# Kernel optimization log

Hardware: AMD Instinct MI355X
Metric: run time of the kernel (lower is better)

The kernel has to match this reference:

```python
import jax, jax.numpy as jnp
import numpy as np

RBF_RADIUS = 12.0
NUM_GAUSSIANS = 50
NUM_ELEMENTS = 100
NUM_MASKS = 1
NUM_HEADS = 8
N_NODES = 50000
N_EDGES = 1000000


def setup_inputs() -> dict:
    key = jax.random.key(0)
    k1, k2, k3, k4 = jax.random.split(key, 4)
    anum = jax.random.randint(k1, (N_NODES,), 0, NUM_ELEMENTS)
    edge_index = jax.random.randint(k2, (2, N_EDGES), 0, N_NODES)
    dist = jax.random.uniform(k3, (N_EDGES,), dtype=jnp.float32) * RBF_RADIUS
    embedding = jax.random.normal(
        k4, (NUM_ELEMENTS, NUM_ELEMENTS, NUM_MASKS, NUM_HEADS, NUM_GAUSSIANS),
        dtype=jnp.float32)
    return {"anum": anum, "edge_index": edge_index, "dist": dist,
            "embedding": embedding}


def _gaussian_smearing(dist):
    # offsets evenly spaced on [0, rbf_radius], std = rbf_radius / num_gaussians
    offsets = jnp.linspace(0.0, RBF_RADIUS, NUM_GAUSSIANS, dtype=jnp.float32)
    std = RBF_RADIUS / NUM_GAUSSIANS
    coeff = -0.5 / (std * std)
    diff = dist[:, None] - offsets[None, :]          # [E, G]
    return jnp.exp(coeff * diff * diff)              # [E, G]


def reference(anum, edge_index, dist, embedding):
    rbf = _gaussian_smearing(dist)                   # [E, G]
    src = anum[edge_index[0]]                        # [E]
    dst = anum[edge_index[1]]                        # [E]
    alphas = embedding[src, dst]                     # [E, M, H, G]
    # einsum 'ijkl,il->jik': i=edges, j=masks, k=heads, l=gaussians
    attn_bias = jnp.einsum('emhg,eg->meh', alphas, rbf)  # [M, E, H]
    return attn_bias
```

## Files before the change

kernel.cpp:

```cpp
#include <hip/hip_runtime.h>


#define G_NUM 50
#define H_NUM 8
#define NE_NUM 100
#define N_PAIRS (NE_NUM * NE_NUM)
#define WIN 16
#define BLOCK_THREADS 256
#define EDGES_PER_BLOCK 128

#define SPACING (12.0f / (float)(G_NUM - 1))
#define INV_SPACING ((float)(G_NUM - 1) / 12.0f)
#define RBF_COEFF (-0.5f * ((float)G_NUM / 12.0f) * ((float)G_NUM / 12.0f))

__global__ __launch_bounds__(BLOCK_THREADS) void transpose_cast_kernel(
    const float* __restrict__ emb, unsigned short* __restrict__ temb)
{
    int idx = blockIdx.x * BLOCK_THREADS + threadIdx.x;
    if (idx < N_PAIRS * H_NUM * G_NUM) {
        int p = idx / (H_NUM * G_NUM);
        int r = idx - p * (H_NUM * G_NUM);
        int g = r >> 3;
        int h = r & 7;
        float f = emb[p * (H_NUM * G_NUM) + h * G_NUM + g];
        unsigned u = __float_as_uint(f);
        unsigned rnd = (u + 0x7fffu + ((u >> 16) & 1u)) >> 16;
        temb[idx] = (unsigned short)rnd;
    }
}

__global__ __launch_bounds__(BLOCK_THREADS) void gather_kernel(
    const int* __restrict__ anum,
    const int* __restrict__ edge_index,
    const float* __restrict__ dist,
    const unsigned short* __restrict__ temb,
    float* __restrict__ out,
    int n_edges)
{
    __shared__ int   pb_s[EDGES_PER_BLOCK];
    __shared__ float dv_s[EDGES_PER_BLOCK];

    const int tid = threadIdx.x;
    const int e0  = blockIdx.x * EDGES_PER_BLOCK;

    if (tid < EDGES_PER_BLOCK) {
        int e = e0 + tid;
        if (e >= n_edges) e = n_edges - 1;
        int s = edge_index[e];
        int d = edge_index[n_edges + e];
        pb_s[tid] = (anum[s] * NE_NUM + anum[d]) * (H_NUM * G_NUM);
        dv_s[tid] = dist[e];
    }
    __syncthreads();

    const int el = tid >> 1;
    const int j  = tid & 1;
    const float dv = dv_s[el];

    int g0 = (int)(dv * INV_SPACING) - 7;
    if (g0 < 0) g0 = 0;
    if (g0 > G_NUM - WIN) g0 = G_NUM - WIN;

    const unsigned short* wb = temb + pb_s[el] + g0 * H_NUM;

    float a0 = 0.f, a1 = 0.f, a2 = 0.f, a3 = 0.f;
    float a4 = 0.f, a5 = 0.f, a6 = 0.f, a7 = 0.f;
    #pragma unroll
    for (int k = 0; k < WIN / 2; ++k) {
        int row = 2 * k + j;
        uint4 v = *(const uint4*)(wb + row * H_NUM);
        float diff = dv - (float)(g0 + row) * SPACING;
        float rb = __expf(RBF_COEFF * diff * diff);
        a0 += rb * __uint_as_float(v.x << 16);
        a1 += rb * __uint_as_float(v.x & 0xffff0000u);
        a2 += rb * __uint_as_float(v.y << 16);
        a3 += rb * __uint_as_float(v.y & 0xffff0000u);
        a4 += rb * __uint_as_float(v.z << 16);
        a5 += rb * __uint_as_float(v.z & 0xffff0000u);
        a6 += rb * __uint_as_float(v.w << 16);
        a7 += rb * __uint_as_float(v.w & 0xffff0000u);
    }

    a0 += __shfl_xor(a0, 1); a1 += __shfl_xor(a1, 1);
    a2 += __shfl_xor(a2, 1); a3 += __shfl_xor(a3, 1);
    a4 += __shfl_xor(a4, 1); a5 += __shfl_xor(a5, 1);
    a6 += __shfl_xor(a6, 1); a7 += __shfl_xor(a7, 1);

    int e = e0 + el;
    if (e < n_edges) {
        float4 w = j ? make_float4(a4, a5, a6, a7) : make_float4(a0, a1, a2, a3);
        *(float4*)(out + (size_t)e * H_NUM + 4 * j) = w;
    }
}

__global__ __launch_bounds__(BLOCK_THREADS) void direct_kernel(
    const int* __restrict__ anum,
    const int* __restrict__ edge_index,
    const float* __restrict__ dist,
    const float* __restrict__ emb,
    float* __restrict__ out,
    int n_edges)
{
    __shared__ int   pair_s[32];
    __shared__ float dist_sd[32];
    __shared__ float rbf_sd[32 * G_NUM];

    const int tid = threadIdx.x;
    const int e0  = blockIdx.x * 32;

    if (tid < 32) {
        int e = e0 + tid;
        if (e >= n_edges) e = n_edges - 1;
        int s  = edge_index[e];
        int d  = edge_index[n_edges + e];
        pair_s[tid] = (anum[s] * NE_NUM + anum[d]) * (H_NUM * G_NUM);
        dist_sd[tid] = dist[e];
    }
    __syncthreads();

    for (int idx = tid; idx < 32 * G_NUM; idx += BLOCK_THREADS) {
        int el = idx / G_NUM;
        int g  = idx - el * G_NUM;
        float diff = dist_sd[el] - (float)g * SPACING;
        rbf_sd[idx] = __expf(RBF_COEFF * diff * diff);
    }
    __syncthreads();

    const int el = tid >> 3;
    const int h  = tid & 7;
    const float* ebase = emb + pair_s[el] + h * G_NUM;
    const float* rbase = rbf_sd + el * G_NUM;

    float acc = 0.0f;
    #pragma unroll
    for (int g2 = 0; g2 < G_NUM / 2; ++g2) {
        float2 ev = *(const float2*)(ebase + 2 * g2);
        float2 rv = *(const float2*)(rbase + 2 * g2);
        acc += ev.x * rv.x + ev.y * rv.y;
    }

    if (e0 + el < n_edges)
        out[e0 * H_NUM + tid] = acc;
}

extern "C" void kernel_launch(void* const* d_in, const int* in_sizes, int n_in,
                              void* d_out, int out_size, void* d_ws, size_t ws_size,
                              hipStream_t stream) {
    const int*   anum       = (const int*)d_in[0];
    const int*   edge_index = (const int*)d_in[1];
    const float* dist       = (const float*)d_in[2];
    const float* emb        = (const float*)d_in[3];
    float*       out        = (float*)d_out;
    const int n_edges = in_sizes[2];

    const size_t temb_bytes = (size_t)N_PAIRS * H_NUM * G_NUM * sizeof(unsigned short);

    if (ws_size < temb_bytes) {
        const int grid = (n_edges + 31) / 32;
        direct_kernel<<<grid, BLOCK_THREADS, 0, stream>>>(
            anum, edge_index, dist, emb, out, n_edges);
        return;
    }

    unsigned short* temb = (unsigned short*)d_ws;

    const int tgrid = (N_PAIRS * H_NUM * G_NUM + BLOCK_THREADS - 1) / BLOCK_THREADS;
    transpose_cast_kernel<<<tgrid, BLOCK_THREADS, 0, stream>>>(emb, temb);

    const int grid = (n_edges + EDGES_PER_BLOCK - 1) / EDGES_PER_BLOCK;
    gather_kernel<<<grid, BLOCK_THREADS, 0, stream>>>(
        anum, edge_index, dist, temb, out, n_edges);
}
```

Baseline: 131.5 us.

## Narrow gaussian window, use one thread per edge, stage transpose through shared memory

The truncated gaussian window in the gather shrinks from 16 to 8 rows. Each thread now handles a whole edge and loads all 8 rows up front, which removes the per-edge thread pair and the shuffle reduction. The transpose-and-cast kernel now stages 8 pairs per block in shared memory with coalesced float4 reads and writes two packed bf16 values per 32-bit store, replacing the strided global reads. The narrower window drops gaussian terms about 3.5 standard deviations out, adding a small approximation error on top of the bf16 rounding.

```diff
diff --git a/kernel.cpp b/kernel.cpp
--- a/kernel.cpp
+++ b/kernel.cpp
@@ -5,27 +5,45 @@
 #define H_NUM 8
 #define NE_NUM 100
 #define N_PAIRS (NE_NUM * NE_NUM)
-#define WIN 16
+#define WIN 8
 #define BLOCK_THREADS 256
-#define EDGES_PER_BLOCK 128
+#define TP_PAIRS 8
 
 #define SPACING (12.0f / (float)(G_NUM - 1))
 #define INV_SPACING ((float)(G_NUM - 1) / 12.0f)
 #define RBF_COEFF (-0.5f * ((float)G_NUM / 12.0f) * ((float)G_NUM / 12.0f))
 
+__device__ __forceinline__ float bf_lo(unsigned u) { return __uint_as_float(u << 16); }
+__device__ __forceinline__ float bf_hi(unsigned u) { return __uint_as_float(u & 0xffff0000u); }
+
 __global__ __launch_bounds__(BLOCK_THREADS) void transpose_cast_kernel(
-    const float* __restrict__ emb, unsigned short* __restrict__ temb)
+    const float* __restrict__ emb, unsigned int* __restrict__ temb)
 {
-    int idx = blockIdx.x * BLOCK_THREADS + threadIdx.x;
-    if (idx < N_PAIRS * H_NUM * G_NUM) {
-        int p = idx / (H_NUM * G_NUM);
-        int r = idx - p * (H_NUM * G_NUM);
-        int g = r >> 3;
-        int h = r & 7;
-        float f = emb[p * (H_NUM * G_NUM) + h * G_NUM + g];
-        unsigned u = __float_as_uint(f);
-        unsigned rnd = (u + 0x7fffu + ((u >> 16) & 1u)) >> 16;
-        temb[idx] = (unsigned short)rnd;
+    __shared__ float ls[TP_PAIRS * H_NUM * G_NUM];
+
+    const int tid = threadIdx.x;
+    const int p0  = blockIdx.x * TP_PAIRS;
+
+    const float4* src = (const float4*)(emb + (size_t)p0 * (H_NUM * G_NUM));
+    #pragma unroll
+    for (int i = tid; i < TP_PAIRS * H_NUM * G_NUM / 4; i += BLOCK_THREADS)
+        ((float4*)ls)[i] = src[i];
+    __syncthreads();
+
+    unsigned int* dst = temb + (size_t)p0 * (H_NUM * G_NUM / 2);
+    #pragma unroll
+    for (int i = tid; i < TP_PAIRS * H_NUM * G_NUM / 2; i += BLOCK_THREADS) {
+        int q  = i / (H_NUM * G_NUM / 2);
+        int u  = i - q * (H_NUM * G_NUM / 2);
+        int g  = u >> 2;
+        int h0 = (u & 3) * 2;
+        float f0 = ls[q * (H_NUM * G_NUM) + h0 * G_NUM + g];
+        float f1 = ls[q * (H_NUM * G_NUM) + (h0 + 1) * G_NUM + g];
+        unsigned u0 = __float_as_uint(f0);
+        unsigned u1 = __float_as_uint(f1);
+        unsigned b0 = (u0 + 0x7fffu + ((u0 >> 16) & 1u)) >> 16;
+        unsigned b1 = (u1 + 0x7fffu + ((u1 >> 16) & 1u)) >> 16;
+        dst[i] = (b1 << 16) | (b0 & 0xffffu);
     }
 }
 
@@ -37,60 +55,44 @@
     float* __restrict__ out,
     int n_edges)
 {
-    __shared__ int   pb_s[EDGES_PER_BLOCK];
-    __shared__ float dv_s[EDGES_PER_BLOCK];
+    int e = blockIdx.x * BLOCK_THREADS + threadIdx.x;
+    if (e >= n_edges) return;
 
-    const int tid = threadIdx.x;
-    const int e0  = blockIdx.x * EDGES_PER_BLOCK;
+    int s = edge_index[e];
+    int d = edge_index[n_edges + e];
+    int p = anum[s] * NE_NUM + anum[d];
+    float dv = dist[e];
 
-    if (tid < EDGES_PER_BLOCK) {
-        int e = e0 + tid;
-        if (e >= n_edges) e = n_edges - 1;
-        int s = edge_index[e];
-        int d = edge_index[n_edges + e];
-        pb_s[tid] = (anum[s] * NE_NUM + anum[d]) * (H_NUM * G_NUM);
-        dv_s[tid] = dist[e];
-    }
-    __syncthreads();
-
-    const int el = tid >> 1;
-    const int j  = tid & 1;
-    const float dv = dv_s[el];
-
-    int g0 = (int)(dv * INV_SPACING) - 7;
+    int g0 = (int)(dv * INV_SPACING) - 3;
     if (g0 < 0) g0 = 0;
     if (g0 > G_NUM - WIN) g0 = G_NUM - WIN;
 
-    const unsigned short* wb = temb + pb_s[el] + g0 * H_NUM;
+    const unsigned short* wb = temb + (size_t)p * (H_NUM * G_NUM) + g0 * H_NUM;
+
+    uint4 v[WIN];
+    #pragma unroll
+    for (int r = 0; r < WIN; ++r)
+        v[r] = *(const uint4*)(wb + r * H_NUM);
 
     float a0 = 0.f, a1 = 0.f, a2 = 0.f, a3 = 0.f;
     float a4 = 0.f, a5 = 0.f, a6 = 0.f, a7 = 0.f;
     #pragma unroll
-    for (int k = 0; k < WIN / 2; ++k) {
-        int row = 2 * k + j;
-        uint4 v = *(const uint4*)(wb + row * H_NUM);
-        float diff = dv - (float)(g0 + row) * SPACING;
+    for (int r = 0; r < WIN; ++r) {
+        float diff = dv - (float)(g0 + r) * SPACING;
         float rb = __expf(RBF_COEFF * diff * diff);
-        a0 += rb * __uint_as_float(v.x << 16);
-        a1 += rb * __uint_as_float(v.x & 0xffff0000u);
-        a2 += rb * __uint_as_float(v.y << 16);
-        a3 += rb * __uint_as_float(v.y & 0xffff0000u);
-        a4 += rb * __uint_as_float(v.z << 16);
-        a5 += rb * __uint_as_float(v.z & 0xffff0000u);
-        a6 += rb * __uint_as_float(v.w << 16);
-        a7 += rb * __uint_as_float(v.w & 0xffff0000u);
+        a0 += rb * bf_lo(v[r].x);
+        a1 += rb * bf_hi(v[r].x);
+        a2 += rb * bf_lo(v[r].y);
+        a3 += rb * bf_hi(v[r].y);
+        a4 += rb * bf_lo(v[r].z);
+        a5 += rb * bf_hi(v[r].z);
+        a6 += rb * bf_lo(v[r].w);
+        a7 += rb * bf_hi(v[r].w);
     }
 
-    a0 += __shfl_xor(a0, 1); a1 += __shfl_xor(a1, 1);
-    a2 += __shfl_xor(a2, 1); a3 += __shfl_xor(a3, 1);
-    a4 += __shfl_xor(a4, 1); a5 += __shfl_xor(a5, 1);
-    a6 += __shfl_xor(a6, 1); a7 += __shfl_xor(a7, 1);
-
-    int e = e0 + el;
-    if (e < n_edges) {
-        float4 w = j ? make_float4(a4, a5, a6, a7) : make_float4(a0, a1, a2, a3);
-        *(float4*)(out + (size_t)e * H_NUM + 4 * j) = w;
-    }
+    float* ob = out + (size_t)e * H_NUM;
+    *(float4*)(ob)     = make_float4(a0, a1, a2, a3);
+    *(float4*)(ob + 4) = make_float4(a4, a5, a6, a7);
 }
 
 __global__ __launch_bounds__(BLOCK_THREADS) void direct_kernel(
@@ -162,12 +164,11 @@
         return;
     }
 
-    unsigned short* temb = (unsigned short*)d_ws;
+    unsigned int* temb = (unsigned int*)d_ws;
 
-    const int tgrid = (N_PAIRS * H_NUM * G_NUM + BLOCK_THREADS - 1) / BLOCK_THREADS;
-    transpose_cast_kernel<<<tgrid, BLOCK_THREADS, 0, stream>>>(emb, temb);
+    transpose_cast_kernel<<<N_PAIRS / TP_PAIRS, BLOCK_THREADS, 0, stream>>>(emb, temb);
 
-    const int grid = (n_edges + EDGES_PER_BLOCK - 1) / EDGES_PER_BLOCK;
+    const int grid = (n_edges + BLOCK_THREADS - 1) / BLOCK_THREADS;
     gather_kernel<<<grid, BLOCK_THREADS, 0, stream>>>(
-        anum, edge_index, dist, temb, out, n_edges);
+        anum, edge_index, dist, (const unsigned short*)temb, out, n_edges);
 }
```

Measured after the change: 112.8 us. -14.2%, faster.
